# Kernel tuning notes

Measured on AMD Instinct MI355X. Metric: run time of the kernel, lower is better.

Reference implementation:

```python
import jax, jax.numpy as jnp
import numpy as np

N_HEAD = 16


def setup_inputs() -> dict:
    key = jax.random.key(0)
    k1, k2, k3 = jax.random.split(key, 3)
    B, T, C = 2, 2048, 1024
    x = jax.random.normal(k1, (B, T, C), dtype=jnp.float32)
    attention_mask = jnp.zeros((B, 1, 1, T), dtype=jnp.float32)
    W_attn = jax.random.normal(k2, (C, 3 * C), dtype=jnp.float32) * 0.02
    b_attn = jnp.zeros((3 * C,), dtype=jnp.float32)
    W_proj = jax.random.normal(k3, (C, C), dtype=jnp.float32) * 0.02
    b_proj = jnp.zeros((C,), dtype=jnp.float32)
    return {"x": x, "attention_mask": attention_mask, "W_attn": W_attn,
            "b_attn": b_attn, "W_proj": W_proj, "b_proj": b_proj}


def reference(x, attention_mask, W_attn, b_attn, W_proj, b_proj):
    B, T, C = x.shape
    H = N_HEAD
    d = C // H
    qkv = x @ W_attn + b_attn                      # [B, T, 3C]
    q, k, v = jnp.split(qkv, 3, axis=-1)
    q = q.reshape(B, T, H, d).transpose(0, 2, 1, 3)  # [B, H, T, d]
    k = k.reshape(B, T, H, d).transpose(0, 2, 1, 3)
    v = v.reshape(B, T, H, d).transpose(0, 2, 1, 3)
    att = jnp.einsum('bhtd,bhsd->bhts', q, k) * (1.0 / np.sqrt(d))
    causal = jnp.tril(jnp.ones((T, T), dtype=bool))
    att = jnp.where(causal[None, None], att, jnp.float32(-10000.0))
    att = att + attention_mask                     # additive broadcast mask
    att = jax.nn.softmax(att, axis=-1)             # dropout p=0.0 -> identity
    y = jnp.einsum('bhts,bhsd->bhtd', att, v)      # [B, H, T, d]
    y = y.transpose(0, 2, 1, 3).reshape(B, T, C)
    return y @ W_proj + b_proj
```

## Files before the change

### kernel.cpp

```cpp
#include <hip/hip_runtime.h>
#include <hip/hip_bf16.h>
#include <stdint.h>

#define BATCH 2
#define TT 2048
#define CC 1024
#define NH 16
#define HD 64

typedef __attribute__((ext_vector_type(8))) short short8;
typedef __attribute__((ext_vector_type(4))) short sh4;
typedef __attribute__((ext_vector_type(4))) float f32x4;
typedef __attribute__((ext_vector_type(2))) unsigned uint2v;

#define MFMA16 __builtin_amdgcn_mfma_f32_16x16x32_bf16
#define LOG2E 1.4426950408889634f

#if defined(__has_builtin)
#if __has_builtin(__builtin_amdgcn_exp2f)
#define EXP2(x) __builtin_amdgcn_exp2f(x)
#else
#define EXP2(x) __expf((x) * 0.6931471805599453f)
#endif
#else
#define EXP2(x) __expf((x) * 0.6931471805599453f)
#endif

__device__ __forceinline__ short f2bf(float f) {
  union { float f; unsigned u; } x;
  x.f = f;
  unsigned r = x.u + 0x7FFFu + ((x.u >> 16) & 1u);
  return (short)(r >> 16);
}

__device__ __forceinline__ void transpose_cast_tile(
    const float* __restrict__ W, short* __restrict__ Wt, int K, int N,
    int n0, int k0, int tid) {
  __shared__ __align__(16) float Ls[64][68];
  {
    const int r = tid >> 4, c4 = (tid & 15) * 4;
#pragma unroll
    for (int p = 0; p < 4; ++p) {
      const float4 v = *reinterpret_cast<const float4*>(
          &W[(size_t)(k0 + r + p * 16) * N + n0 + c4]);
      *reinterpret_cast<float4*>(&Ls[r + p * 16][c4]) = v;
    }
  }
  __syncthreads();
  {
    const int n = tid >> 2;
    const int kk0 = (tid & 3) * 16;
#pragma unroll
    for (int half = 0; half < 2; ++half) {
      short8 o;
#pragma unroll
      for (int t = 0; t < 8; ++t) o[t] = f2bf(Ls[kk0 + half * 8 + t][n]);
      *reinterpret_cast<short8*>(&Wt[(size_t)(n0 + n) * K + k0 + kk0 + half * 8]) = o;
    }
  }
}

__global__ __launch_bounds__(256) void prep_fused(
    const float* __restrict__ x, short* __restrict__ xb,
    const float* __restrict__ W_attn, short* __restrict__ wat,
    const float* __restrict__ W_proj, short* __restrict__ wpt) {
  const int blk = blockIdx.x;
  const int tid = threadIdx.x;
  if (blk < 2048) {
    const int i = (blk * 256 + tid) * 8;
    const float4 a = *reinterpret_cast<const float4*>(&x[i]);
    const float4 b = *reinterpret_cast<const float4*>(&x[i + 4]);
    short8 o;
    o[0] = f2bf(a.x); o[1] = f2bf(a.y); o[2] = f2bf(a.z); o[3] = f2bf(a.w);
    o[4] = f2bf(b.x); o[5] = f2bf(b.y); o[6] = f2bf(b.z); o[7] = f2bf(b.w);
    *reinterpret_cast<short8*>(&xb[i]) = o;
  } else if (blk < 2816) {
    const int b2 = blk - 2048;
    transpose_cast_tile(W_attn, wat, CC, 3 * CC, (b2 % 48) * 64,
                        (b2 / 48) * 64, tid);
  } else {
    const int b3 = blk - 2816;
    transpose_cast_tile(W_proj, wpt, CC, CC, (b3 % 16) * 64, (b3 / 16) * 64,
                        tid);
  }
}

template <bool OUT_BF16>
__device__ __forceinline__ void gemm_bt_body(
    const short* __restrict__ A, const short* __restrict__ Bt,
    const float* __restrict__ bias, void* __restrict__ C,
    short* __restrict__ vT, int M, int N, int K, int QS) {
  __shared__ __align__(16) short SM[12288];
  short* As = SM;
  short* Bs = SM + 4096;
  const int tid = threadIdx.x;
  const int w = tid >> 6, lane = tid & 63;
  const int quad = lane >> 4, l15 = lane & 15;
  const int m0 = blockIdx.y * 64, n0 = blockIdx.x * 128;

  f32x4 acc[4][2] = {};
  const int row16 = lane >> 2;
  const int c4 = (lane & 3) * 8;

  for (int k0 = 0; k0 < K; k0 += 64) {
    __syncthreads();
    {
      const int rbaseA = __builtin_amdgcn_readfirstlane(w * 16);
#pragma unroll
      for (int kh = 0; kh < 2; ++kh) {
        const short* ga = &A[(size_t)(m0 + rbaseA + row16) * K + k0 + kh * 32 + c4];
        __builtin_amdgcn_global_load_lds(
            (const __attribute__((address_space(1))) void*)ga,
            (__attribute__((address_space(3))) void*)&As[kh * 2048 + rbaseA * 32],
            16, 0, 0);
      }
    }
#pragma unroll
    for (int p = 0; p < 2; ++p) {
      const int rbase = __builtin_amdgcn_readfirstlane((w * 2 + p) * 16);
#pragma unroll
      for (int kh = 0; kh < 2; ++kh) {
        const short* gb = &Bt[(size_t)(n0 + rbase + row16) * K + k0 + kh * 32 + c4];
        __builtin_amdgcn_global_load_lds(
            (const __attribute__((address_space(1))) void*)gb,
            (__attribute__((address_space(3))) void*)&Bs[kh * 4096 + rbase * 32],
            16, 0, 0);
      }
    }
    __syncthreads();

    short8 af[2][4], bfr[2][2];
#pragma unroll
    for (int kh = 0; kh < 2; ++kh) {
#pragma unroll
      for (int i = 0; i < 4; ++i)
        af[kh][i] = *reinterpret_cast<const short8*>(
            &As[kh * 2048 + (i * 16 + l15) * 32 + quad * 8]);
#pragma unroll
      for (int j = 0; j < 2; ++j)
        bfr[kh][j] = *reinterpret_cast<const short8*>(
            &Bs[kh * 4096 + (w * 32 + j * 16 + l15) * 32 + quad * 8]);
    }
#pragma unroll
    for (int kh = 0; kh < 2; ++kh)
#pragma unroll
      for (int i = 0; i < 4; ++i)
#pragma unroll
        for (int j = 0; j < 2; ++j)
          acc[i][j] = MFMA16(af[kh][i], bfr[kh][j], acc[i][j], 0, 0, 0);
  }

  if (OUT_BF16 && vT != nullptr && n0 >= 2 * CC) {
    const int n0v = n0 - 2 * CC;
    const int b = m0 >> 11;
    const int s_batch = m0 & (TT - 1);
    short* Ls = SM;
    __syncthreads();
#pragma unroll
    for (int i = 0; i < 4; ++i) {
#pragma unroll
      for (int j = 0; j < 2; ++j) {
        const int dl = w * 32 + j * 16 + l15;
        const int sl = i * 16 + quad * 4;
        const float bb = bias[n0 + dl];
        sh4 pw;
#pragma unroll
        for (int r = 0; r < 4; ++r) pw[r] = f2bf(acc[i][j][r] + bb);
        *reinterpret_cast<sh4*>(&Ls[dl * 88 + sl]) = pw;
      }
    }
    __syncthreads();
    {
      const int row = tid >> 1, seg = tid & 1;
      const int bh = b * 16 + (n0v >> 6) + (row >> 6);
      const int d = row & 63;
      const short8* src = reinterpret_cast<const short8*>(&Ls[row * 88 + seg * 32]);
      short8* dst = reinterpret_cast<short8*>(
          &vT[((size_t)(bh * HD + d)) * TT + s_batch + seg * 32]);
#pragma unroll
      for (int t = 0; t < 4; ++t) dst[t] = src[t];
    }
    return;
  }

#pragma unroll
  for (int i = 0; i < 4; ++i) {
#pragma unroll
    for (int r = 0; r < 4; ++r) {
      const int row = m0 + i * 16 + quad * 4 + r;
#pragma unroll
      for (int j = 0; j < 2; ++j) {
        const int col = n0 + w * 32 + j * 16 + l15;
        float v = acc[i][j][r] + bias[col];
        if (col < QS) v *= 0.18033688011112042f;
        if (OUT_BF16)
          ((short*)C)[(size_t)row * N + col] = f2bf(v);
        else
          ((float*)C)[(size_t)row * N + col] = v;
      }
    }
  }
}

__global__ __launch_bounds__(256) void gemm_qkv(
    const short* __restrict__ A, const short* __restrict__ Bt,
    const float* __restrict__ bias, void* __restrict__ C,
    short* __restrict__ vT, int M, int N, int K, int QS) {
  gemm_bt_body<true>(A, Bt, bias, C, vT, M, N, K, QS);
}

__global__ __launch_bounds__(256) void gemm_proj(
    const short* __restrict__ A, const short* __restrict__ Bt,
    const float* __restrict__ bias, void* __restrict__ C, int M, int N,
    int K) {
  gemm_bt_body<false>(A, Bt, bias, C, nullptr, M, N, K, 0);
}

#define PST 72
__global__ __launch_bounds__(256) void attn_mfma8(
    const short* __restrict__ qkv, const short* __restrict__ vT,
    const float* __restrict__ mask, short* __restrict__ y) {
  __shared__ __align__(16) short Ks[2][64 * PST];
  __shared__ __align__(16) short Vs[2][64 * PST];
  __shared__ __align__(16) short Ps[64 * PST];
  const int tid = threadIdx.x;
  const int w = tid >> 6, lane = tid & 63;
  const int quad = lane >> 4, l15 = lane & 15;
  const int bh = blockIdx.y, b = bh >> 4, h = bh & 15;
  const int px = blockIdx.x;
  const int qh = 31 - px;
  const int nth = qh + 1;
  const int ntot = nth + px + 1;
  const int RS = 3 * CC;

  int qt = qh;
  int qrow0 = qt * 64 + w * 16;

  short8 qf0, qf1;
  {
    const size_t qrow = (size_t)(b * TT + qrow0 + l15) * RS + h * HD + quad * 8;
    qf0 = *reinterpret_cast<const short8*>(&qkv[qrow]);
    qf1 = *reinterpret_cast<const short8*>(&qkv[qrow + 32]);
  }

  float l_run = 0.f;
  f32x4 o_acc[4] = {};

  const int sr = tid >> 3, sc = (tid & 7) * 8;
  const short* kbase = qkv + (size_t)(b * TT + sr) * RS + CC + h * HD + sc;
  const short* vbase = vT + (size_t)(bh * HD + sr) * TT + sc;
  const float* mptr = mask + b * TT + quad * 4;
  short* psrow = &Ps[(w * 16 + l15) * PST];
  const int kfo0 = quad * 8, kfo1 = 32 + quad * 8;

  short8 kpre0 = *reinterpret_cast<const short8*>(kbase);
  short8 kpre1 = *reinterpret_cast<const short8*>(kbase + (size_t)32 * RS);
  short8 vpre0 = *reinterpret_cast<const short8*>(vbase);
  short8 vpre1 = *reinterpret_cast<const short8*>(vbase + 32 * TT);

  for (int it = 0; it < ntot; ++it) {
    const int kt = (it < nth) ? it : it - nth;
    const int s0 = kt * 64;

    f32x4 mv[4];
#pragma unroll
    for (int j = 0; j < 4; ++j)
      mv[j] = *reinterpret_cast<const f32x4*>(&mptr[s0 + j * 16]);

    if (it == nth) {
#pragma unroll
      for (int r = 0; r < 4; ++r) {
        const float lr = __shfl(l_run, quad * 4 + r, 64);
        const float inv = 1.0f / lr;
        const size_t row = (size_t)(b * TT + qrow0 + quad * 4 + r);
#pragma unroll
        for (int t = 0; t < 4; ++t)
          y[row * CC + h * HD + t * 16 + l15] = f2bf(o_acc[t][r] * inv);
      }
      qt = px;
      qrow0 = qt * 64 + w * 16;
      const size_t qrow = (size_t)(b * TT + qrow0 + l15) * RS + h * HD + quad * 8;
      qf0 = *reinterpret_cast<const short8*>(&qkv[qrow]);
      qf1 = *reinterpret_cast<const short8*>(&qkv[qrow + 32]);
      l_run = 0.f;
#pragma unroll
      for (int t = 0; t < 4; ++t) o_acc[t] = f32x4{0.f, 0.f, 0.f, 0.f};
    }

    const int cur = it & 1;
    *reinterpret_cast<short8*>(&Ks[cur][sr * PST + sc]) = kpre0;
    *reinterpret_cast<short8*>(&Ks[cur][(sr + 32) * PST + sc]) = kpre1;
    *reinterpret_cast<short8*>(&Vs[cur][sr * PST + sc]) = vpre0;
    *reinterpret_cast<short8*>(&Vs[cur][(sr + 32) * PST + sc]) = vpre1;
    __syncthreads();

    if (it + 1 < ntot) {
      const int ktn = (it + 1 == nth) ? 0 : kt + 1;
      const short* kp = kbase + (size_t)ktn * 64 * RS;
      const short* vp = vbase + ktn * 64;
      kpre0 = *reinterpret_cast<const short8*>(kp);
      kpre1 = *reinterpret_cast<const short8*>(kp + (size_t)32 * RS);
      vpre0 = *reinterpret_cast<const short8*>(vp);
      vpre1 = *reinterpret_cast<const short8*>(vp + 32 * TT);
    }

    f32x4 sa[4] = {};
#pragma unroll
    for (int j = 0; j < 4; ++j) {
      const short8 kf0 = *reinterpret_cast<const short8*>(
          &Ks[cur][(j * 16 + l15) * PST + kfo0]);
      const short8 kf1 = *reinterpret_cast<const short8*>(
          &Ks[cur][(j * 16 + l15) * PST + kfo1]);
      sa[j] = MFMA16(kf0, qf0, sa[j], 0, 0, 0);
      sa[j] = MFMA16(kf1, qf1, sa[j], 0, 0, 0);
    }

    float rs = 0.f;
    const bool boundary = (kt == qt);
    const int qg = qrow0 + l15;
#pragma unroll
    for (int j = 0; j < 4; ++j) {
      float pv[4];
#pragma unroll
      for (int r = 0; r < 4; ++r) {
        float v = __builtin_fmaf(mv[j][r], LOG2E, sa[j][r]);
        if (boundary) {
          const int sg = s0 + j * 16 + quad * 4 + r;
          if (sg > qg) v = -10000.0f;
        }
        pv[r] = EXP2(v);
      }
      union { __hip_bfloat162 h2[2]; uint2v u; } pk;
      pk.h2[0] = __float22bfloat162_rn(make_float2(pv[0], pv[1]));
      pk.h2[1] = __float22bfloat162_rn(make_float2(pv[2], pv[3]));
      *reinterpret_cast<uint2v*>(&psrow[j * 16 + quad * 4]) = pk.u;
      rs += (pv[0] + pv[1]) + (pv[2] + pv[3]);
    }
    rs += __shfl_xor(rs, 16, 64);
    rs += __shfl_xor(rs, 32, 64);
    l_run += rs;

    const short8 pf0 = *reinterpret_cast<const short8*>(&psrow[kfo0]);
    const short8 pf1 = *reinterpret_cast<const short8*>(&psrow[kfo1]);
#pragma unroll
    for (int t = 0; t < 4; ++t) {
      const short8 vf0 = *reinterpret_cast<const short8*>(
          &Vs[cur][(t * 16 + l15) * PST + kfo0]);
      const short8 vf1 = *reinterpret_cast<const short8*>(
          &Vs[cur][(t * 16 + l15) * PST + kfo1]);
      o_acc[t] = MFMA16(pf0, vf0, o_acc[t], 0, 0, 0);
      o_acc[t] = MFMA16(pf1, vf1, o_acc[t], 0, 0, 0);
    }
  }

#pragma unroll
  for (int r = 0; r < 4; ++r) {
    const float lr = __shfl(l_run, quad * 4 + r, 64);
    const float inv = 1.0f / lr;
    const size_t row = (size_t)(b * TT + qrow0 + quad * 4 + r);
#pragma unroll
    for (int t = 0; t < 4; ++t)
      y[row * CC + h * HD + t * 16 + l15] = f2bf(o_acc[t][r] * inv);
  }
}

extern "C" void kernel_launch(void* const* d_in, const int* in_sizes, int n_in,
                              void* d_out, int out_size, void* d_ws,
                              size_t ws_size, hipStream_t stream) {
  const float* x = (const float*)d_in[0];
  const float* attn_mask = (const float*)d_in[1];
  const float* W_attn = (const float*)d_in[2];
  const float* b_attn = (const float*)d_in[3];
  const float* W_proj = (const float*)d_in[4];
  const float* b_proj = (const float*)d_in[5];
  float* out = (float*)d_out;

  const int M = BATCH * TT;

  short* xb = (short*)d_ws;
  short* wat = xb + (size_t)M * CC;
  short* wpt = wat + (size_t)(3 * CC) * CC;
  short* qkvb = wpt + (size_t)CC * CC;
  short* yb = qkvb + (size_t)M * 3 * CC;
  short* vTb = yb + (size_t)M * CC;

  prep_fused<<<3072, 256, 0, stream>>>(x, xb, W_attn, wat, W_proj, wpt);

  gemm_qkv<<<dim3((3 * CC) / 128, M / 64), 256, 0, stream>>>(
      xb, wat, b_attn, qkvb, vTb, M, 3 * CC, CC, CC);

  attn_mfma8<<<dim3(16, BATCH * NH), 256, 0, stream>>>(
      qkvb, vTb, attn_mask, yb);

  gemm_proj<<<dim3(CC / 128, M / 64), 256, 0, stream>>>(
      yb, wpt, b_proj, out, M, CC, CC);
}
```

Before: 194.2 us.

## Drop paired query-tile scheduling for one tile per block; add MFMA setprio hints

The attention kernel used to process two query tiles per block (qh and 31-qh) so every block did the same amount of causal work. It now launches 32 blocks per head, each handling a single query tile, which doubles the grid and per-block work ranges from 1 to 32 key tiles. It also raises wave priority around the two MFMA loops with s_setprio. This trades load balance for more parallelism and simpler control flow, at the risk of a tail of long-running blocks.

```diff
diff --git a/kernel.cpp b/kernel.cpp
--- a/kernel.cpp
+++ b/kernel.cpp
@@ -217,7 +217,7 @@
 }
 
 #define PST 72
-__global__ __launch_bounds__(256) void attn_mfma8(
+__global__ __launch_bounds__(256) void attn_mfma9(
     const short* __restrict__ qkv, const short* __restrict__ vT,
     const float* __restrict__ mask, short* __restrict__ y) {
   __shared__ __align__(16) short Ks[2][64 * PST];
@@ -227,14 +227,11 @@
   const int w = tid >> 6, lane = tid & 63;
   const int quad = lane >> 4, l15 = lane & 15;
   const int bh = blockIdx.y, b = bh >> 4, h = bh & 15;
-  const int px = blockIdx.x;
-  const int qh = 31 - px;
-  const int nth = qh + 1;
-  const int ntot = nth + px + 1;
+  const int qt = 31 - blockIdx.x;
+  const int nkt = qt + 1;
   const int RS = 3 * CC;
 
-  int qt = qh;
-  int qrow0 = qt * 64 + w * 16;
+  const int qrow0 = qt * 64 + w * 16;
 
   short8 qf0, qf1;
   {
@@ -258,34 +255,13 @@
   short8 vpre0 = *reinterpret_cast<const short8*>(vbase);
   short8 vpre1 = *reinterpret_cast<const short8*>(vbase + 32 * TT);
 
-  for (int it = 0; it < ntot; ++it) {
-    const int kt = (it < nth) ? it : it - nth;
-    const int s0 = kt * 64;
+  for (int it = 0; it < nkt; ++it) {
+    const int s0 = it * 64;
 
     f32x4 mv[4];
 #pragma unroll
     for (int j = 0; j < 4; ++j)
       mv[j] = *reinterpret_cast<const f32x4*>(&mptr[s0 + j * 16]);
-
-    if (it == nth) {
-#pragma unroll
-      for (int r = 0; r < 4; ++r) {
-        const float lr = __shfl(l_run, quad * 4 + r, 64);
-        const float inv = 1.0f / lr;
-        const size_t row = (size_t)(b * TT + qrow0 + quad * 4 + r);
-#pragma unroll
-        for (int t = 0; t < 4; ++t)
-          y[row * CC + h * HD + t * 16 + l15] = f2bf(o_acc[t][r] * inv);
-      }
-      qt = px;
-      qrow0 = qt * 64 + w * 16;
-      const size_t qrow = (size_t)(b * TT + qrow0 + l15) * RS + h * HD + quad * 8;
-      qf0 = *reinterpret_cast<const short8*>(&qkv[qrow]);
-      qf1 = *reinterpret_cast<const short8*>(&qkv[qrow + 32]);
-      l_run = 0.f;
-#pragma unroll
-      for (int t = 0; t < 4; ++t) o_acc[t] = f32x4{0.f, 0.f, 0.f, 0.f};
-    }
 
     const int cur = it & 1;
     *reinterpret_cast<short8*>(&Ks[cur][sr * PST + sc]) = kpre0;
@@ -294,10 +270,9 @@
     *reinterpret_cast<short8*>(&Vs[cur][(sr + 32) * PST + sc]) = vpre1;
     __syncthreads();
 
-    if (it + 1 < ntot) {
-      const int ktn = (it + 1 == nth) ? 0 : kt + 1;
-      const short* kp = kbase + (size_t)ktn * 64 * RS;
-      const short* vp = vbase + ktn * 64;
+    if (it + 1 < nkt) {
+      const short* kp = kbase + (size_t)(it + 1) * 64 * RS;
+      const short* vp = vbase + (it + 1) * 64;
       kpre0 = *reinterpret_cast<const short8*>(kp);
       kpre1 = *reinterpret_cast<const short8*>(kp + (size_t)32 * RS);
       vpre0 = *reinterpret_cast<const short8*>(vp);
@@ -305,6 +280,7 @@
     }
 
     f32x4 sa[4] = {};
+    __builtin_amdgcn_s_setprio(1);
 #pragma unroll
     for (int j = 0; j < 4; ++j) {
       const short8 kf0 = *reinterpret_cast<const short8*>(
@@ -314,9 +290,10 @@
       sa[j] = MFMA16(kf0, qf0, sa[j], 0, 0, 0);
       sa[j] = MFMA16(kf1, qf1, sa[j], 0, 0, 0);
     }
+    __builtin_amdgcn_s_setprio(0);
 
     float rs = 0.f;
-    const bool boundary = (kt == qt);
+    const bool boundary = (it == qt);
     const int qg = qrow0 + l15;
 #pragma unroll
     for (int j = 0; j < 4; ++j) {
@@ -342,6 +319,7 @@
 
     const short8 pf0 = *reinterpret_cast<const short8*>(&psrow[kfo0]);
     const short8 pf1 = *reinterpret_cast<const short8*>(&psrow[kfo1]);
+    __builtin_amdgcn_s_setprio(1);
 #pragma unroll
     for (int t = 0; t < 4; ++t) {
       const short8 vf0 = *reinterpret_cast<const short8*>(
@@ -351,6 +329,7 @@
       o_acc[t] = MFMA16(pf0, vf0, o_acc[t], 0, 0, 0);
       o_acc[t] = MFMA16(pf1, vf1, o_acc[t], 0, 0, 0);
     }
+    __builtin_amdgcn_s_setprio(0);
   }
 
 #pragma unroll
@@ -389,7 +368,7 @@
   gemm_qkv<<<dim3((3 * CC) / 128, M / 64), 256, 0, stream>>>(
       xb, wat, b_attn, qkvb, vTb, M, 3 * CC, CC, CC);
 
-  attn_mfma8<<<dim3(16, BATCH * NH), 256, 0, stream>>>(
+  attn_mfma9<<<dim3(32, BATCH * NH), 256, 0, stream>>>(
       qkvb, vTb, attn_mask, yb);
 
   gemm_proj<<<dim3(CC / 128, M / 64), 256, 0, stream>>>(
```

Measured after the change: 217.5 us. 1.12x slower.

## Double-buffer GEMM LDS tiles to overlap global loads with MFMA

Applied to the files above, without the earlier changes.

Doubles the shared-memory buffer in the bf16 GEMM body so the next K tile is loaded asynchronously via global_load_lds while the current tile is consumed by MFMAs. Each iteration now has one barrier instead of two. This aims to hide global-memory latency behind compute, at the cost of twice the LDS per block, which may lower occupancy.

```diff
diff --git a/kernel.cpp b/kernel.cpp
--- a/kernel.cpp
+++ b/kernel.cpp
@@ -90,9 +90,9 @@
     const short* __restrict__ A, const short* __restrict__ Bt,
     const float* __restrict__ bias, void* __restrict__ C,
     short* __restrict__ vT, int M, int N, int K, int QS) {
-  __shared__ __align__(16) short SM[12288];
+  __shared__ __align__(16) short SM[24576];
   short* As = SM;
-  short* Bs = SM + 4096;
+  short* Bs = SM + 8192;
   const int tid = threadIdx.x;
   const int w = tid >> 6, lane = tid & 63;
   const int quad = lane >> 4, l15 = lane & 15;
@@ -102,32 +102,43 @@
   const int row16 = lane >> 2;
   const int c4 = (lane & 3) * 8;
 
+  const int rbaseA = __builtin_amdgcn_readfirstlane(w * 16);
+  const int rbaseB0 = __builtin_amdgcn_readfirstlane(w * 2 * 16);
+  const int rbaseB1 = __builtin_amdgcn_readfirstlane((w * 2 + 1) * 16);
+
+#define STAGE_TILE(buf, k0)                                                    \
+  {                                                                            \
+    _Pragma("unroll") for (int kh = 0; kh < 2; ++kh) {                         \
+      const short* ga =                                                        \
+          &A[(size_t)(m0 + rbaseA + row16) * K + (k0) + kh * 32 + c4];         \
+      __builtin_amdgcn_global_load_lds(                                        \
+          (const __attribute__((address_space(1))) void*)ga,                   \
+          (__attribute__((address_space(3))) void*)                            \
+              &As[(buf)*4096 + kh * 2048 + rbaseA * 32],                       \
+          16, 0, 0);                                                           \
+      const short* gb0 =                                                       \
+          &Bt[(size_t)(n0 + rbaseB0 + row16) * K + (k0) + kh * 32 + c4];       \
+      __builtin_amdgcn_global_load_lds(                                        \
+          (const __attribute__((address_space(1))) void*)gb0,                  \
+          (__attribute__((address_space(3))) void*)                            \
+              &Bs[(buf)*8192 + kh * 4096 + rbaseB0 * 32],                      \
+          16, 0, 0);                                                           \
+      const short* gb1 =                                                       \
+          &Bt[(size_t)(n0 + rbaseB1 + row16) * K + (k0) + kh * 32 + c4];       \
+      __builtin_amdgcn_global_load_lds(                                        \
+          (const __attribute__((address_space(1))) void*)gb1,                  \
+          (__attribute__((address_space(3))) void*)                            \
+              &Bs[(buf)*8192 + kh * 4096 + rbaseB1 * 32],                      \
+          16, 0, 0);                                                           \
+    }                                                                          \
+  }
+
+  STAGE_TILE(0, 0)
+  __syncthreads();
+
+  int cur = 0;
   for (int k0 = 0; k0 < K; k0 += 64) {
-    __syncthreads();
-    {
-      const int rbaseA = __builtin_amdgcn_readfirstlane(w * 16);
-#pragma unroll
-      for (int kh = 0; kh < 2; ++kh) {
-        const short* ga = &A[(size_t)(m0 + rbaseA + row16) * K + k0 + kh * 32 + c4];
-        __builtin_amdgcn_global_load_lds(
-            (const __attribute__((address_space(1))) void*)ga,
-            (__attribute__((address_space(3))) void*)&As[kh * 2048 + rbaseA * 32],
-            16, 0, 0);
-      }
-    }
-#pragma unroll
-    for (int p = 0; p < 2; ++p) {
-      const int rbase = __builtin_amdgcn_readfirstlane((w * 2 + p) * 16);
-#pragma unroll
-      for (int kh = 0; kh < 2; ++kh) {
-        const short* gb = &Bt[(size_t)(n0 + rbase + row16) * K + k0 + kh * 32 + c4];
-        __builtin_amdgcn_global_load_lds(
-            (const __attribute__((address_space(1))) void*)gb,
-            (__attribute__((address_space(3))) void*)&Bs[kh * 4096 + rbase * 32],
-            16, 0, 0);
-      }
-    }
-    __syncthreads();
+    if (k0 + 64 < K) STAGE_TILE(cur ^ 1, k0 + 64)
 
     short8 af[2][4], bfr[2][2];
 #pragma unroll
@@ -135,11 +146,12 @@
 #pragma unroll
       for (int i = 0; i < 4; ++i)
         af[kh][i] = *reinterpret_cast<const short8*>(
-            &As[kh * 2048 + (i * 16 + l15) * 32 + quad * 8]);
+            &As[cur * 4096 + kh * 2048 + (i * 16 + l15) * 32 + quad * 8]);
 #pragma unroll
       for (int j = 0; j < 2; ++j)
         bfr[kh][j] = *reinterpret_cast<const short8*>(
-            &Bs[kh * 4096 + (w * 32 + j * 16 + l15) * 32 + quad * 8]);
+            &Bs[cur * 8192 + kh * 4096 + (w * 32 + j * 16 + l15) * 32 +
+                quad * 8]);
     }
 #pragma unroll
     for (int kh = 0; kh < 2; ++kh)
@@ -148,14 +160,17 @@
 #pragma unroll
         for (int j = 0; j < 2; ++j)
           acc[i][j] = MFMA16(af[kh][i], bfr[kh][j], acc[i][j], 0, 0, 0);
-  }
+
+    __syncthreads();
+    cur ^= 1;
+  }
+#undef STAGE_TILE
 
   if (OUT_BF16 && vT != nullptr && n0 >= 2 * CC) {
     const int n0v = n0 - 2 * CC;
     const int b = m0 >> 11;
     const int s_batch = m0 & (TT - 1);
     short* Ls = SM;
-    __syncthreads();
 #pragma unroll
     for (int i = 0; i < 4; ++i) {
 #pragma unroll
```

New measurement: 184.0 us. -5.3%, faster.
